# Kernel tuning notes

Hardware: AMD Instinct MI355X
Metric: run time of the kernel (lower is better)

The kernel has to match this reference:

```python
import jax, jax.numpy as jnp
import numpy as np

D_MODEL = 1024
D_STATE = 16
EXPAND = 2
D_CONV = 4
D_INNER = EXPAND * D_MODEL          # 2048
DT_RANK = D_MODEL // 16             # 64
B = 2
L = 1024
EPS = 1e-5


def setup_inputs() -> dict:
    key = jax.random.key(0)
    ks = jax.random.split(key, 8)
    s = 0.02
    return {
        "x": jax.random.normal(ks[0], (B, L, D_MODEL), jnp.float32),
        "ln_gamma": jnp.ones((D_MODEL,), jnp.float32),
        "ln_beta": jnp.zeros((D_MODEL,), jnp.float32),
        "in_proj_w": jax.random.normal(ks[1], (2 * D_INNER, D_MODEL), jnp.float32) * s,
        "conv_w": jax.random.normal(ks[2], (D_INNER, 1, D_CONV), jnp.float32) * s,
        "conv_b": jnp.zeros((D_INNER,), jnp.float32),
        "x_proj_w": jax.random.normal(ks[3], (DT_RANK + 2 * D_STATE, D_INNER), jnp.float32) * s,
        "dt_proj_w": jax.random.normal(ks[4], (D_INNER, DT_RANK), jnp.float32) * s,
        "dt_proj_b": jax.random.normal(ks[5], (D_INNER,), jnp.float32) * 0.01,
        "A_log": jnp.log(jnp.tile(jnp.arange(1, D_STATE + 1, dtype=jnp.float32), (D_INNER, 1))),
        "D_skip": jnp.ones((D_INNER,), jnp.float32),
        "out_proj_w": jax.random.normal(ks[6], (D_MODEL, D_INNER), jnp.float32) * s,
    }


def _layernorm(x, g, b):
    mu = jnp.mean(x, axis=-1, keepdims=True)
    var = jnp.mean((x - mu) ** 2, axis=-1, keepdims=True)
    return (x - mu) * jax.lax.rsqrt(var + EPS) * g + b


def _mamba_forward(x, ln_gamma, ln_beta, in_proj_w, conv_w, conv_b,
                   x_proj_w, dt_proj_w, dt_proj_b, A_log, D_skip, out_proj_w):
    residual = x
    xn = _layernorm(x, ln_gamma, ln_beta)

    # in_proj -> split into ssm input u and gate z   (b, l, 2*d_inner)
    xz = jnp.einsum('bld,ed->ble', xn, in_proj_w)
    u, z = jnp.split(xz, 2, axis=-1)

    # causal depthwise conv1d (padding = d_conv-1 on the left, truncated to L)
    uc = jnp.transpose(u, (0, 2, 1))  # (b, d_inner, l)
    uc = jax.lax.conv_general_dilated(
        uc, conv_w, window_strides=(1,), padding=[(D_CONV - 1, 0)],
        feature_group_count=D_INNER,
        dimension_numbers=('NCH', 'OIH', 'NCH'))
    uc = uc + conv_b[None, :, None]
    u = jax.nn.silu(jnp.transpose(uc, (0, 2, 1)))  # (b, l, d_inner)

    # selective SSM
    A = -jnp.exp(A_log)                              # (d_inner, d_state)
    x_dbl = jnp.einsum('bld,ed->ble', u, x_proj_w)   # (b, l, dt_rank+2*n)
    dt, Bm, Cm = jnp.split(x_dbl, [DT_RANK, DT_RANK + D_STATE], axis=-1)
    delta = jax.nn.softplus(jnp.einsum('blr,dr->bld', dt, dt_proj_w) + dt_proj_b)

    def step(h, inputs):
        d_t, B_t, C_t, u_t = inputs            # (b,di) (b,n) (b,n) (b,di)
        dA = jnp.exp(d_t[..., None] * A)       # (b, di, n)
        h = dA * h + (d_t * u_t)[..., None] * B_t[:, None, :]
        y = jnp.einsum('bdn,bn->bd', h, C_t)
        return h, y

    h0 = jnp.zeros((x.shape[0], D_INNER, D_STATE), x.dtype)
    xs = (jnp.moveaxis(delta, 1, 0), jnp.moveaxis(Bm, 1, 0),
          jnp.moveaxis(Cm, 1, 0), jnp.moveaxis(u, 1, 0))
    _, ys = jax.lax.scan(step, h0, xs)
    y = jnp.moveaxis(ys, 0, 1) + u * D_skip     # (b, l, d_inner)

    y = y * jax.nn.silu(z)                      # gated output
    out = jnp.einsum('ble,de->bld', y, out_proj_w)
    # dropout is identity in eval mode
    return out + residual


def reference(x, ln_gamma, ln_beta, in_proj_w, conv_w, conv_b,
              x_proj_w, dt_proj_w, dt_proj_b, A_log, D_skip, out_proj_w):
    return _mamba_forward(x, ln_gamma, ln_beta, in_proj_w, conv_w, conv_b,
                          x_proj_w, dt_proj_w, dt_proj_b, A_log, D_skip, out_proj_w)
```

## Files before the change

kernel.cpp:

```cpp
#include <hip/hip_runtime.h>

#define D_MODEL 1024
#define D_STATE 16
#define D_INNER 2048
#define DT_RANK 64
#define NBATCH 2
#define SEQ_L 1024
#define M_ROWS (NBATCH * SEQ_L)
#define CHUNK 64
#define NCHUNK (SEQ_L / CHUNK)

typedef __bf16 bf16x8 __attribute__((ext_vector_type(8)));
typedef float f32x4 __attribute__((ext_vector_type(4)));
typedef unsigned short u16;
typedef unsigned int u32;

__device__ __forceinline__ float bf2f(u16 h) {
    return __uint_as_float(((unsigned)h) << 16);
}
__device__ __forceinline__ u16 f2bf(float f) {
    unsigned u = __float_as_uint(f);
    u += 0x7fff + ((u >> 16) & 1);
    return (u16)(u >> 16);
}

__global__ __launch_bounds__(256) void cast_all(
    const float* __restrict__ s0, const float* __restrict__ s1,
    const float* __restrict__ s2, const float* __restrict__ s3,
    u16* __restrict__ d0, u16* __restrict__ d1,
    u16* __restrict__ d2, u16* __restrict__ d3) {
    int idx = blockIdx.x * 256 + threadIdx.x;
    if (idx < 4194304) {
        d0[idx] = f2bf(s0[idx]);
    } else if (idx < 6291456) {
        int i = idx - 4194304; d1[i] = f2bf(s1[i]);
    } else if (idx < 6488064) {
        int i = idx - 6291456; d2[i] = f2bf(s2[i]);
    } else {
        int i = idx - 6488064; d3[i] = f2bf(s3[i]);
    }
}

__global__ __launch_bounds__(256) void ln_kernel(
    const float* __restrict__ x, const float* __restrict__ g,
    const float* __restrict__ b, u16* __restrict__ xn) {
    int row = blockIdx.x;
    const float4* xr = (const float4*)(x + (size_t)row * D_MODEL);
    float4 v = xr[threadIdx.x];
    float s  = v.x + v.y + v.z + v.w;
    float ss = v.x * v.x + v.y * v.y + v.z * v.z + v.w * v.w;
#pragma unroll
    for (int off = 32; off > 0; off >>= 1) {
        s  += __shfl_down(s,  off, 64);
        ss += __shfl_down(ss, off, 64);
    }
    __shared__ float sh_s[4], sh_ss[4];
    int wid = threadIdx.x >> 6;
    if ((threadIdx.x & 63) == 0) { sh_s[wid] = s; sh_ss[wid] = ss; }
    __syncthreads();
    float mu  = (sh_s[0] + sh_s[1] + sh_s[2] + sh_s[3]) * (1.0f / D_MODEL);
    float var = (sh_ss[0] + sh_ss[1] + sh_ss[2] + sh_ss[3]) * (1.0f / D_MODEL) - mu * mu;
    float rs = rsqrtf(var + 1e-5f);
    int c0 = threadIdx.x * 4;
    float vv[4] = {v.x, v.y, v.z, v.w};
#pragma unroll
    for (int j = 0; j < 4; j++) {
        int c = c0 + j;
        float o = (vv[j] - mu) * rs * g[c] + b[c];
        xn[(size_t)row * D_MODEL + c] = f2bf(o);
    }
}

template <int BM, int BN, int WM, int WN, int MODE>
__global__ __launch_bounds__(256) void gemm_lds(
    const __bf16* __restrict__ A, const __bf16* __restrict__ W,
    int K, int ldC,
    float* __restrict__ outF, u16* __restrict__ outB,
    const float* __restrict__ auxF) {
    constexpr int WCOLS = BN / (WN * 16);
    __shared__ __bf16 As[BM * 32];
    __shared__ __bf16 Bs[BN * 32];
    int tid  = threadIdx.x;
    int lane = tid & 63;
    int wid  = tid >> 6;
    int l16  = lane & 15;
    int quad = lane >> 4;
    int wr = wid / WCOLS;
    int wc = wid % WCOLS;
    int m0 = blockIdx.y * BM;
    int n0 = blockIdx.x * BN;

    f32x4 acc[WM][WN];
#pragma unroll
    for (int mi = 0; mi < WM; mi++)
#pragma unroll
        for (int nj = 0; nj < WN; nj++)
            acc[mi][nj] = (f32x4){0.f, 0.f, 0.f, 0.f};

    for (int k0 = 0; k0 < K; k0 += 32) {
        __syncthreads();
#pragma unroll
        for (int i = 0; i < BM / 64; i++) {
            int t   = i * 256 + tid;
            int row = t >> 2;
            int cg  = (t & 3) ^ ((row >> 1) & 3);
            __builtin_amdgcn_global_load_lds(
                (const __attribute__((address_space(1))) u32*)(A + (size_t)(m0 + row) * K + k0 + cg * 8),
                (__attribute__((address_space(3))) u32*)(As + (i * 256 + wid * 64) * 8),
                16, 0, 0);
        }
#pragma unroll
        for (int i = 0; i < BN / 64; i++) {
            int t   = i * 256 + tid;
            int row = t >> 2;
            int cg  = (t & 3) ^ ((row >> 1) & 3);
            __builtin_amdgcn_global_load_lds(
                (const __attribute__((address_space(1))) u32*)(W + (size_t)(n0 + row) * K + k0 + cg * 8),
                (__attribute__((address_space(3))) u32*)(Bs + (i * 256 + wid * 64) * 8),
                16, 0, 0);
        }
        __syncthreads();

        bf16x8 af[WM], bfr[WN];
#pragma unroll
        for (int mi = 0; mi < WM; mi++) {
            int r  = wr * WM * 16 + mi * 16 + l16;
            int cg = quad ^ ((r >> 1) & 3);
            af[mi] = *(const bf16x8*)(As + r * 32 + cg * 8);
        }
#pragma unroll
        for (int nj = 0; nj < WN; nj++) {
            int r  = wc * WN * 16 + nj * 16 + l16;
            int cg = quad ^ ((r >> 1) & 3);
            bfr[nj] = *(const bf16x8*)(Bs + r * 32 + cg * 8);
        }
#pragma unroll
        for (int mi = 0; mi < WM; mi++)
#pragma unroll
            for (int nj = 0; nj < WN; nj++)
                acc[mi][nj] = __builtin_amdgcn_mfma_f32_16x16x32_bf16(
                    af[mi], bfr[nj], acc[mi][nj], 0, 0, 0);
    }

#pragma unroll
    for (int mi = 0; mi < WM; mi++) {
#pragma unroll
        for (int nj = 0; nj < WN; nj++) {
            int col = n0 + wc * WN * 16 + nj * 16 + l16;
#pragma unroll
            for (int r = 0; r < 4; r++) {
                int row = m0 + wr * WM * 16 + mi * 16 + quad * 4 + r;
                float v = acc[mi][nj][r];
                if (MODE == 0) {
                    outB[(size_t)row * ldC + col] = f2bf(v);
                } else {
                    outF[(size_t)row * ldC + col] = v + auxF[(size_t)row * ldC + col];
                }
            }
        }
    }
}

template <int MODE>
__global__ __launch_bounds__(256) void gemm_bt(
    const __bf16* __restrict__ A, const __bf16* __restrict__ W,
    int K, int Ksplit, int Nw, int ldC,
    float* __restrict__ outF, const float* __restrict__ auxF) {
    int lane = threadIdx.x & 63;
    int wid  = threadIdx.x >> 6;
    int m0 = blockIdx.y * 64;
    int n0 = blockIdx.x * 64;
    int kc = blockIdx.z;
    int l16  = lane & 15;
    int quad = lane >> 4;
    int mrow = m0 + wid * 16 + l16;

    const __bf16* ap = A + (size_t)mrow * K + kc * Ksplit + quad * 8;
    const __bf16* wp[4];
#pragma unroll
    for (int j = 0; j < 4; j++) {
        int nc = n0 + j * 16 + l16;
        if (nc > Nw - 1) nc = Nw - 1;
        wp[j] = W + (size_t)nc * K + kc * Ksplit + quad * 8;
    }
    f32x4 acc[4];
#pragma unroll
    for (int j = 0; j < 4; j++) acc[j] = (f32x4){0.f, 0.f, 0.f, 0.f};

    for (int k = 0; k < Ksplit; k += 32) {
        bf16x8 a = *(const bf16x8*)ap;
        ap += 32;
#pragma unroll
        for (int j = 0; j < 4; j++) {
            bf16x8 bfr = *(const bf16x8*)wp[j];
            wp[j] += 32;
            acc[j] = __builtin_amdgcn_mfma_f32_16x16x32_bf16(a, bfr, acc[j], 0, 0, 0);
        }
    }
    float* out = (MODE == 1) ? outF + (size_t)kc * (M_ROWS * 96) : outF;
#pragma unroll
    for (int j = 0; j < 4; j++) {
        int col = n0 + j * 16 + l16;
#pragma unroll
        for (int r = 0; r < 4; r++) {
            int row = m0 + wid * 16 + quad * 4 + r;
            float v = acc[j][r];
            if (MODE == 1) {
                if (col < Nw) out[(size_t)row * ldC + col] = v;
            } else {
                float t = v + auxF[col];
                float sp = (t > 20.f) ? t : log1pf(__expf(t));
                out[(size_t)row * ldC + col] = sp;
            }
        }
    }
}

__global__ __launch_bounds__(256) void xdbl_reduce(
    const float* __restrict__ xdp, float* __restrict__ xd) {
    int idx = blockIdx.x * 256 + threadIdx.x;
    const int N = M_ROWS * 96;
    xd[idx] = xdp[idx] + xdp[idx + N] + xdp[idx + 2 * N] + xdp[idx + 3 * N];
}

__global__ __launch_bounds__(256) void conv_silu(
    const u16* __restrict__ xz, const float* __restrict__ cw,
    const float* __restrict__ cb, u16* __restrict__ uc) {
    int idx = blockIdx.x * 256 + threadIdx.x;
    int d = idx & (D_INNER - 1);
    int m = idx >> 11;
    int t = m & (SEQ_L - 1);
    float s = cb[d];
#pragma unroll
    for (int j = 0; j < 4; j++) {
        int tt = t - 3 + j;
        if (tt >= 0) {
            s += cw[d * 4 + j] *
                 bf2f(xz[(size_t)(m - 3 + j) * (2 * D_INNER) + d]);
        }
    }
    float sig = 1.f / (1.f + __expf(-s));
    uc[idx] = f2bf(s * sig);
}

__global__ __launch_bounds__(256) void cast_dt(
    const float* __restrict__ xd, u16* __restrict__ dtb) {
    int idx = blockIdx.x * 256 + threadIdx.x;
    int mrow = idx >> 6;
    int r = idx & 63;
    dtb[idx] = f2bf(xd[(size_t)mrow * 96 + r]);
}


__global__ __launch_bounds__(256) void scan_chunk(
    const float* __restrict__ delta, const u16* __restrict__ uc,
    const float* __restrict__ xd, const float* __restrict__ A_log,
    float* __restrict__ Pst, float* __restrict__ Sst) {
    __shared__ float Bsh[CHUNK][16];
    int tid  = threadIdx.x;
    int lane = tid & 63;
    int w    = tid >> 6;
    int dsub = lane & 15;
    int g    = lane >> 4;
    int n0   = g * 4;
    int c = blockIdx.x, b = blockIdx.z;
    int d = blockIdx.y * 64 + w * 16 + dsub;
    int mbase = b * SEQ_L + c * CHUNK;

    {
        int row = tid >> 2, q = tid & 3;
        *(float4*)&Bsh[row][q * 4] =
            *(const float4*)(xd + (size_t)(mbase + row) * 96 + DT_RANK + q * 4);
    }
    __syncthreads();

    float a[4];
    {
        float4 a0 = *(const float4*)(A_log + d * D_STATE + n0);
        a[0] = -__expf(a0.x); a[1] = -__expf(a0.y);
        a[2] = -__expf(a0.z); a[3] = -__expf(a0.w);
    }
    float P[4] = {1.f, 1.f, 1.f, 1.f}, S[4] = {0.f, 0.f, 0.f, 0.f};

    for (int t0 = 0; t0 < CHUNK; t0 += 4) {
        float dlv[4], uv[4];
#pragma unroll
        for (int i = 0; i < 4; i++) {
            int m = mbase + t0 + i;
            dlv[i] = delta[(size_t)m * D_INNER + d];
            uv[i]  = bf2f(uc[(size_t)m * D_INNER + d]);
        }
#pragma unroll
        for (int i = 0; i < 4; i++) {
            float c1 = dlv[i] * uv[i];
#pragma unroll
            for (int j = 0; j < 4; j++) {
                float dA = __expf(dlv[i] * a[j]);
                P[j] *= dA;
                S[j] = dA * S[j] + c1 * Bsh[t0 + i][n0 + j];
            }
        }
    }
    size_t s = ((size_t)(b * D_INNER + d) * NCHUNK + c) * D_STATE + n0;
    *(float4*)(Pst + s) = (float4){P[0], P[1], P[2], P[3]};
    *(float4*)(Sst + s) = (float4){S[0], S[1], S[2], S[3]};
}

__global__ __launch_bounds__(256) void scan_combine(
    const float* __restrict__ Pst, const float* __restrict__ Sst,
    float* __restrict__ Hin) {
    int idx = blockIdx.x * 256 + threadIdx.x;
    int bd = idx >> 4;
    int n  = idx & 15;
    float h = 0.f;
#pragma unroll
    for (int c = 0; c < NCHUNK; ++c) {
        size_t s = ((size_t)bd * NCHUNK + c) * D_STATE + n;
        Hin[s] = h;
        h = Pst[s] * h + Sst[s];
    }
}

__global__ __launch_bounds__(256) void scan_apply(
    const float* __restrict__ delta, const u16* __restrict__ uc,
    const float* __restrict__ xd, const u16* __restrict__ xz,
    const float* __restrict__ A_log, const float* __restrict__ Dsk,
    const float* __restrict__ Hin, u16* __restrict__ yg) {
    __shared__ float BCs[CHUNK][32];
    int tid  = threadIdx.x;
    int lane = tid & 63;
    int w    = tid >> 6;
    int dsub = lane & 15;
    int g    = lane >> 4;
    int n0   = g * 4;
    int c = blockIdx.x, b = blockIdx.z;
    int d = blockIdx.y * 64 + w * 16 + dsub;
    int mbase = b * SEQ_L + c * CHUNK;

    {
#pragma unroll
        for (int i = 0; i < 2; i++) {
            int idx = i * 256 + tid;
            int row = idx >> 3, q = idx & 7;
            *(float4*)&BCs[row][q * 4] =
                *(const float4*)(xd + (size_t)(mbase + row) * 96 + DT_RANK + q * 4);
        }
    }
    __syncthreads();

    float a[4];
    {
        float4 a0 = *(const float4*)(A_log + d * D_STATE + n0);
        a[0] = -__expf(a0.x); a[1] = -__expf(a0.y);
        a[2] = -__expf(a0.z); a[3] = -__expf(a0.w);
    }
    float h[4];
    {
        float4 h0 = *(const float4*)(Hin +
            (((size_t)(b * D_INNER + d) * NCHUNK + c) * D_STATE + n0));
        h[0] = h0.x; h[1] = h0.y; h[2] = h0.z; h[3] = h0.w;
    }
    float dsk = Dsk[d];

    for (int t0 = 0; t0 < CHUNK; t0 += 4) {
        float dlv[4], uv[4], zv[4];
#pragma unroll
        for (int i = 0; i < 4; i++) {
            int m = mbase + t0 + i;
            dlv[i] = delta[(size_t)m * D_INNER + d];
            uv[i]  = bf2f(uc[(size_t)m * D_INNER + d]);
            zv[i]  = bf2f(xz[(size_t)m * (2 * D_INNER) + D_INNER + d]);
        }
#pragma unroll
        for (int i = 0; i < 4; i++) {
            int t = t0 + i;
            float c1 = dlv[i] * uv[i];
            float y = 0.f;
#pragma unroll
            for (int j = 0; j < 4; j++) {
                float dA = __expf(dlv[i] * a[j]);
                h[j] = dA * h[j] + c1 * BCs[t][n0 + j];
                y += h[j] * BCs[t][16 + n0 + j];
            }
            y += __shfl_xor(y, 16);
            y += __shfl_xor(y, 32);
            if (g == 0) {
                float z = zv[i];
                float yv = y + uv[i] * dsk;
                float gt = z / (1.f + __expf(-z));
                yg[(size_t)(mbase + t) * D_INNER + d] = f2bf(yv * gt);
            }
        }
    }
}

extern "C" void kernel_launch(void* const* d_in, const int* in_sizes, int n_in,
                              void* d_out, int out_size, void* d_ws, size_t ws_size,
                              hipStream_t stream) {
    const float* x         = (const float*)d_in[0];
    const float* ln_g      = (const float*)d_in[1];
    const float* ln_b      = (const float*)d_in[2];
    const float* in_proj_w = (const float*)d_in[3];
    const float* conv_w    = (const float*)d_in[4];
    const float* conv_b    = (const float*)d_in[5];
    const float* x_proj_w  = (const float*)d_in[6];
    const float* dt_proj_w = (const float*)d_in[7];
    const float* dt_proj_b = (const float*)d_in[8];
    const float* A_log     = (const float*)d_in[9];
    const float* Dsk       = (const float*)d_in[10];
    const float* out_proj_w= (const float*)d_in[11];

    char* ws = (char*)d_ws;
    u16* xn   = (u16*)ws;    ws += (size_t)M_ROWS * D_MODEL * 2;
    u16* xz   = (u16*)ws;    ws += (size_t)M_ROWS * 2 * D_INNER * 2;
    u16* ucv  = (u16*)ws;    ws += (size_t)M_ROWS * D_INNER * 2;
    float* xd = (float*)ws;  ws += (size_t)M_ROWS * 96 * 4;
    u16* dtb  = (u16*)ws;    ws += (size_t)M_ROWS * DT_RANK * 2;
    float* dl = (float*)ws;  ws += (size_t)M_ROWS * D_INNER * 4;
    u16* yg   = (u16*)ws;    ws += (size_t)M_ROWS * D_INNER * 2;
    u16* w_in = (u16*)ws;    ws += (size_t)4194304 * 2;
    u16* w_out= (u16*)ws;    ws += (size_t)2097152 * 2;
    u16* w_xp = (u16*)ws;    ws += (size_t)196608 * 2;
    u16* w_dt = (u16*)ws;

    float* Pst = (float*)w_in;
    float* Sst = (float*)w_in + 1048576;
    float* Hin = (float*)xn;
    float* xdp = (float*)yg;

    cast_all<<<25856, 256, 0, stream>>>(in_proj_w, out_proj_w, x_proj_w, dt_proj_w,
                                        w_in, w_out, w_xp, w_dt);
    ln_kernel<<<M_ROWS, 256, 0, stream>>>(x, ln_g, ln_b, xn);
    gemm_lds<128, 128, 4, 4, 0><<<dim3(4096 / 128, M_ROWS / 128), 256, 0, stream>>>(
        (const __bf16*)xn, (const __bf16*)w_in, D_MODEL, 2 * D_INNER,
        nullptr, xz, nullptr);
    conv_silu<<<(M_ROWS * D_INNER) / 256, 256, 0, stream>>>(xz, conv_w, conv_b, ucv);
    gemm_bt<1><<<dim3(2, 32, 4), 256, 0, stream>>>(
        (const __bf16*)ucv, (const __bf16*)w_xp, D_INNER, D_INNER / 4, 96, 96,
        xdp, nullptr);
    xdbl_reduce<<<(M_ROWS * 96) / 256, 256, 0, stream>>>(xdp, xd);
    cast_dt<<<(M_ROWS * DT_RANK) / 256, 256, 0, stream>>>(xd, dtb);
    gemm_bt<2><<<dim3(32, 32, 1), 256, 0, stream>>>(
        (const __bf16*)dtb, (const __bf16*)w_dt, DT_RANK, DT_RANK, D_INNER,
        D_INNER, dl, dt_proj_b);
    dim3 sgrid(NCHUNK, D_INNER / 64, NBATCH);
    scan_chunk<<<sgrid, 256, 0, stream>>>(dl, ucv, xd, A_log, Pst, Sst);
    scan_combine<<<(NBATCH * D_INNER * D_STATE) / 256, 256, 0, stream>>>(Pst, Sst, Hin);
    scan_apply<<<sgrid, 256, 0, stream>>>(dl, ucv, xd, xz, A_log, Dsk, Hin, yg);
    gemm_lds<64, 128, 4, 2, 3><<<dim3(1024 / 128, M_ROWS / 64), 256, 0, stream>>>(
        (const __bf16*)yg, (const __bf16*)w_out, D_INNER, D_MODEL,
        (float*)d_out, nullptr, x);
}
```

Before: 290.9 us.

## Split-K out_proj GEMM with fused reduce, smaller in_proj tile, fuse dt cast

```diff
diff --git a/kernel.cpp b/kernel.cpp
--- a/kernel.cpp
+++ b/kernel.cpp
@@ -74,9 +74,8 @@
 template <int BM, int BN, int WM, int WN, int MODE>
 __global__ __launch_bounds__(256) void gemm_lds(
     const __bf16* __restrict__ A, const __bf16* __restrict__ W,
-    int K, int ldC,
-    float* __restrict__ outF, u16* __restrict__ outB,
-    const float* __restrict__ auxF) {
+    int K, int Ksteps, int ldC,
+    float* __restrict__ outF, u16* __restrict__ outB) {
     constexpr int WCOLS = BN / (WN * 16);
     __shared__ __bf16 As[BM * 32];
     __shared__ __bf16 Bs[BN * 32];
@@ -89,6 +88,7 @@
     int wc = wid % WCOLS;
     int m0 = blockIdx.y * BM;
     int n0 = blockIdx.x * BN;
+    int kbase = blockIdx.z * Ksteps * 32;
 
     f32x4 acc[WM][WN];
 #pragma unroll
@@ -97,7 +97,8 @@
         for (int nj = 0; nj < WN; nj++)
             acc[mi][nj] = (f32x4){0.f, 0.f, 0.f, 0.f};
 
-    for (int k0 = 0; k0 < K; k0 += 32) {
+    for (int ki = 0; ki < Ksteps; ki++) {
+        int k0 = kbase + ki * 32;
         __syncthreads();
 #pragma unroll
         for (int i = 0; i < BM / 64; i++) {
@@ -142,6 +143,7 @@
                     af[mi], bfr[nj], acc[mi][nj], 0, 0, 0);
     }
 
+    float* outP = (MODE == 4) ? outF + (size_t)blockIdx.z * M_ROWS * ldC : outF;
 #pragma unroll
     for (int mi = 0; mi < WM; mi++) {
 #pragma unroll
@@ -154,11 +156,29 @@
                 if (MODE == 0) {
                     outB[(size_t)row * ldC + col] = f2bf(v);
                 } else {
-                    outF[(size_t)row * ldC + col] = v + auxF[(size_t)row * ldC + col];
+                    outP[(size_t)row * ldC + col] = v;
                 }
             }
         }
     }
+}
+
+__global__ __launch_bounds__(256) void out_reduce(
+    const float* __restrict__ p, const float* __restrict__ x,
+    float* __restrict__ out) {
+    int idx = blockIdx.x * 256 + threadIdx.x;
+    const int N = M_ROWS * D_MODEL;
+    float4 a = ((const float4*)p)[idx];
+    float4 b = ((const float4*)(p + N))[idx];
+    float4 c = ((const float4*)(p + 2 * N))[idx];
+    float4 d = ((const float4*)(p + 3 * N))[idx];
+    float4 r = ((const float4*)x)[idx];
+    float4 o;
+    o.x = a.x + b.x + c.x + d.x + r.x;
+    o.y = a.y + b.y + c.y + d.y + r.y;
+    o.z = a.z + b.z + c.z + d.z + r.z;
+    o.w = a.w + b.w + c.w + d.w + r.w;
+    ((float4*)out)[idx] = o;
 }
 
 template <int MODE>
@@ -217,10 +237,17 @@
 }
 
 __global__ __launch_bounds__(256) void xdbl_reduce(
-    const float* __restrict__ xdp, float* __restrict__ xd) {
+    const float* __restrict__ xdp, float* __restrict__ xd,
+    u16* __restrict__ dtb) {
     int idx = blockIdx.x * 256 + threadIdx.x;
     const int N = M_ROWS * 96;
-    xd[idx] = xdp[idx] + xdp[idx + N] + xdp[idx + 2 * N] + xdp[idx + 3 * N];
+    float v = 0.f;
+#pragma unroll
+    for (int i = 0; i < 8; i++) v += xdp[idx + i * N];
+    xd[idx] = v;
+    int mrow = idx / 96;
+    int r = idx - mrow * 96;
+    if (r < DT_RANK) dtb[mrow * DT_RANK + r] = f2bf(v);
 }
 
 __global__ __launch_bounds__(256) void conv_silu(
@@ -242,15 +269,6 @@
     float sig = 1.f / (1.f + __expf(-s));
     uc[idx] = f2bf(s * sig);
 }
-
-__global__ __launch_bounds__(256) void cast_dt(
-    const float* __restrict__ xd, u16* __restrict__ dtb) {
-    int idx = blockIdx.x * 256 + threadIdx.x;
-    int mrow = idx >> 6;
-    int r = idx & 63;
-    dtb[idx] = f2bf(xd[(size_t)mrow * 96 + r]);
-}
-
 
 __global__ __launch_bounds__(256) void scan_chunk(
     const float* __restrict__ delta, const u16* __restrict__ uc,
@@ -427,19 +445,19 @@
     float* Sst = (float*)w_in + 1048576;
     float* Hin = (float*)xn;
     float* xdp = (float*)yg;
+    float* opart = (float*)xz;
 
     cast_all<<<25856, 256, 0, stream>>>(in_proj_w, out_proj_w, x_proj_w, dt_proj_w,
                                         w_in, w_out, w_xp, w_dt);
     ln_kernel<<<M_ROWS, 256, 0, stream>>>(x, ln_g, ln_b, xn);
-    gemm_lds<128, 128, 4, 4, 0><<<dim3(4096 / 128, M_ROWS / 128), 256, 0, stream>>>(
-        (const __bf16*)xn, (const __bf16*)w_in, D_MODEL, 2 * D_INNER,
-        nullptr, xz, nullptr);
+    gemm_lds<64, 128, 4, 2, 0><<<dim3(4096 / 128, M_ROWS / 64, 1), 256, 0, stream>>>(
+        (const __bf16*)xn, (const __bf16*)w_in, D_MODEL, D_MODEL / 32, 2 * D_INNER,
+        nullptr, xz);
     conv_silu<<<(M_ROWS * D_INNER) / 256, 256, 0, stream>>>(xz, conv_w, conv_b, ucv);
-    gemm_bt<1><<<dim3(2, 32, 4), 256, 0, stream>>>(
-        (const __bf16*)ucv, (const __bf16*)w_xp, D_INNER, D_INNER / 4, 96, 96,
+    gemm_bt<1><<<dim3(2, 32, 8), 256, 0, stream>>>(
+        (const __bf16*)ucv, (const __bf16*)w_xp, D_INNER, D_INNER / 8, 96, 96,
         xdp, nullptr);
-    xdbl_reduce<<<(M_ROWS * 96) / 256, 256, 0, stream>>>(xdp, xd);
-    cast_dt<<<(M_ROWS * DT_RANK) / 256, 256, 0, stream>>>(xd, dtb);
+    xdbl_reduce<<<(M_ROWS * 96) / 256, 256, 0, stream>>>(xdp, xd, dtb);
     gemm_bt<2><<<dim3(32, 32, 1), 256, 0, stream>>>(
         (const __bf16*)dtb, (const __bf16*)w_dt, DT_RANK, DT_RANK, D_INNER,
         D_INNER, dl, dt_proj_b);
@@ -447,7 +465,9 @@
     scan_chunk<<<sgrid, 256, 0, stream>>>(dl, ucv, xd, A_log, Pst, Sst);
     scan_combine<<<(NBATCH * D_INNER * D_STATE) / 256, 256, 0, stream>>>(Pst, Sst, Hin);
     scan_apply<<<sgrid, 256, 0, stream>>>(dl, ucv, xd, xz, A_log, Dsk, Hin, yg);
-    gemm_lds<64, 128, 4, 2, 3><<<dim3(1024 / 128, M_ROWS / 64), 256, 0, stream>>>(
-        (const __bf16*)yg, (const __bf16*)w_out, D_INNER, D_MODEL,
-        (float*)d_out, nullptr, x);
-}
+    gemm_lds<64, 128, 4, 2, 4><<<dim3(1024 / 128, M_ROWS / 64, 4), 256, 0, stream>>>(
+        (const __bf16*)yg, (const __bf16*)w_out, D_INNER, D_INNER / 4 / 32, D_MODEL,
+        opart, nullptr);
+    out_reduce<<<(M_ROWS * D_MODEL / 4) / 256, 256, 0, stream>>>(
+        opart, x, (float*)d_out);
+}
```

New measurement: 273.9 us. 1.06x faster.
